# Kernel optimization log

Hardware: AMD Instinct MI355X
Metric: run time of the kernel (lower is better)

Reference implementation:

```python
import jax, jax.numpy as jnp
import numpy as np

SCALES = (4, 8, 8)
PAD = 2
TOTAL = 256  # prod(SCALES) == frame shift
INDENT = PAD * TOTAL
BN_EPS = 1e-3  # keras BatchNormalization default


def _bn(x, g, b, m, v):
    return (x - m) * jax.lax.rsqrt(v + BN_EPS) * g + b


def _conv1d_valid(x, w):
    # x: [B, T, Cin], w: [K, Cin, Cout]
    return jax.lax.conv_general_dilated(x, w, (1,), 'VALID',
                                         dimension_numbers=('NWC', 'WIO', 'NWC'))


def _mel_conv_same(x, w):
    # per-mel-bin shared 1D conv along time. x: [B, T, M], w: [K]
    B, T, M = x.shape
    lhs = x.transpose(0, 2, 1).reshape(B * M, T, 1)
    rhs = w.reshape(-1, 1, 1)
    y = jax.lax.conv_general_dilated(lhs, rhs, (1,), 'SAME',
                                     dimension_numbers=('NWC', 'WIO', 'NWC'))
    return y.reshape(B, M, T).transpose(0, 2, 1)


def _gru(x, Wx, Wh, bx, bh):
    # keras GRUCell (reset_after=True): gate order z, r, h; h' = z*h + (1-z)*hh
    xp = x @ Wx + bx  # [B, T, 3H], input projection hoisted out of the scan
    H = Wh.shape[0]
    h0 = jnp.zeros((x.shape[0], H), x.dtype)

    def step(h, xt):
        rp = h @ Wh + bh
        xz, xr, xh = jnp.split(xt, 3, axis=-1)
        rz, rr, rh = jnp.split(rp, 3, axis=-1)
        z = jax.nn.sigmoid(xz + rz)
        r = jax.nn.sigmoid(xr + rr)
        hh = jnp.tanh(xh + r * rh)
        hn = z * h + (1.0 - z) * hh
        return hn, hn

    _, ys = jax.lax.scan(step, h0, xp.transpose(1, 0, 2))
    return ys.transpose(1, 0, 2)


def setup_inputs() -> dict:
    key = jax.random.key(0)
    ks = iter(jax.random.split(key, 64))
    B, T_MEL, M, C, H, R = 4, 44, 80, 128, 512, 10
    T_UP = TOTAL * (T_MEL - 2 * PAD)  # 10240
    s = 0.05
    d = {}
    d['audios'] = jax.random.normal(next(ks), (B, T_UP + 1), jnp.float32)
    d['mels'] = jax.random.normal(next(ks), (B, T_MEL, M), jnp.float32)
    d['w_mel0'] = jnp.full((2 * SCALES[0] + 1,), 1.0 / (2 * SCALES[0] + 1), jnp.float32)
    d['w_mel1'] = jnp.full((2 * SCALES[1] + 1,), 1.0 / (2 * SCALES[1] + 1), jnp.float32)
    d['w_mel2'] = jnp.full((2 * SCALES[2] + 1,), 1.0 / (2 * SCALES[2] + 1), jnp.float32)
    d['mr_conv0_w'] = jax.random.normal(next(ks), (5, M, C), jnp.float32) * s
    d['mr_bn0_g'] = jax.random.uniform(next(ks), (C,), jnp.float32, 0.5, 1.5)
    d['mr_bn0_b'] = jax.random.normal(next(ks), (C,), jnp.float32) * s
    d['mr_bn0_m'] = jnp.zeros((C,), jnp.float32)
    d['mr_bn0_v'] = jnp.ones((C,), jnp.float32)
    d['r_w1'] = jax.random.normal(next(ks), (R, C, C), jnp.float32) * s
    d['r_bn1_g'] = jax.random.uniform(next(ks), (R, C), jnp.float32, 0.5, 1.5)
    d['r_bn1_b'] = jax.random.normal(next(ks), (R, C), jnp.float32) * s
    d['r_bn1_m'] = jnp.zeros((R, C), jnp.float32)
    d['r_bn1_v'] = jnp.ones((R, C), jnp.float32)
    d['r_w2'] = jax.random.normal(next(ks), (R, C, C), jnp.float32) * s
    d['r_bn2_g'] = jax.random.uniform(next(ks), (R, C), jnp.float32, 0.5, 1.5)
    d['r_bn2_b'] = jax.random.normal(next(ks), (R, C), jnp.float32) * s
    d['r_bn2_m'] = jnp.zeros((R, C), jnp.float32)
    d['r_bn2_v'] = jnp.ones((R, C), jnp.float32)
    d['mr_out_w'] = jax.random.normal(next(ks), (C, C), jnp.float32) * s
    d['mr_out_b'] = jnp.zeros((C,), jnp.float32)
    A4 = C // 4  # 32
    d['Wi'] = jax.random.normal(next(ks), (1 + M + A4, H), jnp.float32) * s
    d['bi'] = jnp.zeros((H,), jnp.float32)
    d['Wx0'] = jax.random.normal(next(ks), (H, 3 * H), jnp.float32) * s
    d['Wh0'] = jax.random.normal(next(ks), (H, 3 * H), jnp.float32) * s
    d['bx0'] = jnp.zeros((3 * H,), jnp.float32)
    d['bh0'] = jnp.zeros((3 * H,), jnp.float32)
    d['Wx1'] = jax.random.normal(next(ks), (H + A4, 3 * H), jnp.float32) * s
    d['Wh1'] = jax.random.normal(next(ks), (H, 3 * H), jnp.float32) * s
    d['bx1'] = jnp.zeros((3 * H,), jnp.float32)
    d['bh1'] = jnp.zeros((3 * H,), jnp.float32)
    d['Wd0'] = jax.random.normal(next(ks), (H + A4, H), jnp.float32) * s
    d['bd0'] = jnp.zeros((H,), jnp.float32)
    d['Wd1'] = jax.random.normal(next(ks), (H + A4, H), jnp.float32) * s
    d['bd1'] = jnp.zeros((H,), jnp.float32)
    d['Wp'] = jax.random.normal(next(ks), (H, 30), jnp.float32) * s
    d['bp'] = jnp.zeros((30,), jnp.float32)
    return d


def reference(audios, mels, w_mel0, w_mel1, w_mel2,
              mr_conv0_w, mr_bn0_g, mr_bn0_b, mr_bn0_m, mr_bn0_v,
              r_w1, r_bn1_g, r_bn1_b, r_bn1_m, r_bn1_v,
              r_w2, r_bn2_g, r_bn2_b, r_bn2_m, r_bn2_v,
              mr_out_w, mr_out_b, Wi, bi,
              Wx0, Wh0, bx0, bh0, Wx1, Wh1, bx1, bh1,
              Wd0, bd0, Wd1, bd1, Wp, bp):
    # ---- UpsampleNet mel branch: nearest upsample + smoothing conv per scale ----
    x = mels
    for w, scale in zip((w_mel0, w_mel1, w_mel2), SCALES):
        x = jnp.repeat(x, scale, axis=1)
        x = _mel_conv_same(x, w)
    mels_up = x[:, INDENT:-INDENT, :]  # [B, T_up, 80]

    # ---- UpsampleNet aux branch: MelResNet (inference BN) + nearest upsample ----
    a = jax.nn.relu(_bn(_conv1d_valid(mels, mr_conv0_w),
                        mr_bn0_g, mr_bn0_b, mr_bn0_m, mr_bn0_v))
    for i in range(r_w1.shape[0]):
        y = jax.nn.relu(_bn(a @ r_w1[i], r_bn1_g[i], r_bn1_b[i], r_bn1_m[i], r_bn1_v[i]))
        y = _bn(y @ r_w2[i], r_bn2_g[i], r_bn2_b[i], r_bn2_m[i], r_bn2_v[i])
        a = a + y
    a = a @ mr_out_w + mr_out_b
    aux = jnp.repeat(a, TOTAL, axis=1)  # [B, T_up, 128]
    a0, a1, a2, a3 = jnp.split(aux, 4, axis=-1)

    # ---- WaveRNN teacher-forced trunk ----
    x = jnp.concatenate([audios[:, :-1, None], mels_up, a0], axis=-1)
    x = x @ Wi + bi  # [B, T_up, 512]
    x = _gru(x, Wx0, Wh0, bx0, bh0) + x
    x = _gru(jnp.concatenate([x, a1], axis=-1), Wx1, Wh1, bx1, bh1) + x
    x = jax.nn.relu(jnp.concatenate([x, a2], axis=-1) @ Wd0 + bd0) + x
    x = jax.nn.relu(jnp.concatenate([x, a3], axis=-1) @ Wd1 + bd1) + x
    logits = x @ Wp + bp  # [B, T_up, 30] (MoL parameters)
    return logits
```

## Files before the change

kernel.cpp:

```cpp
#include <hip/hip_runtime.h>
#include <hip/hip_bf16.h>

#define T_SEQ 10240
#define GRU_W 8

typedef short bf16x8 __attribute__((ext_vector_type(8)));
typedef float f32x4 __attribute__((ext_vector_type(4)));

__device__ __forceinline__ float bf2f(unsigned short u) {
    return __uint_as_float(((unsigned int)u) << 16);
}

__global__ void upsample_kernel(const float* __restrict__ in, float* __restrict__ out,
                                const float* __restrict__ wk,
                                int B, int Tin, int Tout, int shift, int taps)
{
    int idx = blockIdx.x * blockDim.x + threadIdx.x;
    int total = B * Tout * 80;
    if (idx >= total) return;
    int m = idx % 80;
    int r = idx / 80;
    int t = r % Tout;
    int b = r / Tout;
    int s = taps >> 1;
    float acc = 0.f;
    for (int d = -s; d <= s; ++d) {
        int i = t + d;
        if (i >= 0 && i < Tout)
            acc += in[((size_t)b * Tin + (i >> shift)) * 80 + m] * wk[d + s];
    }
    out[idx] = acc;
}

__global__ __launch_bounds__(128) void conv0_kernel(
    const float* __restrict__ mels, const float* __restrict__ w,
    const float* __restrict__ g, const float* __restrict__ b,
    const float* __restrict__ m_, const float* __restrict__ v_,
    float* __restrict__ a)
{
    __shared__ float xin[400];
    int bt = blockIdx.x;
    int bb = bt / 40, t = bt % 40;
    int c = threadIdx.x;
    for (int idx = c; idx < 400; idx += 128)
        xin[idx] = mels[((size_t)bb * 44 + t + idx / 80) * 80 + (idx % 80)];
    __syncthreads();
    float s = 0.f;
    for (int q = 0; q < 400; ++q) s += xin[q] * w[q * 128 + c];
    s = (s - m_[c]) * rsqrtf(v_[c] + 1e-3f) * g[c] + b[c];
    a[bt * 128 + c] = fmaxf(s, 0.f);
}

__global__ __launch_bounds__(128) void resblock_kernel(
    const float* __restrict__ W1, const float* __restrict__ W2,
    const float* __restrict__ g1, const float* __restrict__ b1,
    const float* __restrict__ m1, const float* __restrict__ v1,
    const float* __restrict__ g2, const float* __restrict__ b2,
    const float* __restrict__ m2, const float* __restrict__ v2,
    float* __restrict__ a)
{
    __shared__ float ain[128], y1[128];
    int tok = blockIdx.x;
    int c = threadIdx.x;
    ain[c] = a[tok * 128 + c];
    __syncthreads();
    float s = 0.f;
    #pragma unroll 8
    for (int k = 0; k < 128; ++k) s += ain[k] * W1[k * 128 + c];
    s = (s - m1[c]) * rsqrtf(v1[c] + 1e-3f) * g1[c] + b1[c];
    y1[c] = fmaxf(s, 0.f);
    __syncthreads();
    float s2 = 0.f;
    #pragma unroll 8
    for (int k = 0; k < 128; ++k) s2 += y1[k] * W2[k * 128 + c];
    s2 = (s2 - m2[c]) * rsqrtf(v2[c] + 1e-3f) * g2[c] + b2[c];
    a[tok * 128 + c] = ain[c] + s2;
}

__global__ __launch_bounds__(128) void outmat_kernel(
    const float* __restrict__ W, const float* __restrict__ bias,
    const float* __restrict__ a, float* __restrict__ out)
{
    __shared__ float ain[128];
    int tok = blockIdx.x;
    int c = threadIdx.x;
    ain[c] = a[tok * 128 + c];
    __syncthreads();
    float s = 0.f;
    #pragma unroll 8
    for (int k = 0; k < 128; ++k) s += ain[k] * W[k * 128 + c];
    out[tok * 128 + c] = s + bias[c];
}

__device__ __forceinline__ float fetchA(int mode, int row, int k, int K,
    const float* audio, const float* melsup, const float* cond, const float* xA)
{
    if (k >= K) return 0.f;
    int b = row / T_SEQ;
    int t = row - b * T_SEQ;
    if (mode == 0) {
        if (k == 0) return audio[(size_t)b * (T_SEQ + 1) + t];
        if (k < 81) return melsup[((size_t)b * 11264 + 512 + t) * 80 + (k - 1)];
        return cond[((size_t)b * 40 + (t >> 8)) * 128 + (k - 81)];
    }
    if (k < 512) return xA[(size_t)row * 512 + k];
    int co = (mode == 2) ? 32 : (mode == 3) ? 64 : 96;
    return cond[((size_t)b * 40 + (t >> 8)) * 128 + co + (k - 512)];
}

__global__ __launch_bounds__(256) void gemm_big(
    int mode, int N, int K,
    const float* __restrict__ W, const float* __restrict__ bias1,
    const float* __restrict__ bias2,
    const float* __restrict__ audio, const float* __restrict__ melsup,
    const float* __restrict__ cond, const float* __restrict__ xA,
    const float* __restrict__ resid, float* __restrict__ outF,
    __hip_bfloat16* __restrict__ outB)
{
    __shared__ float As[16][68];
    __shared__ float Bs[16][68];
    const int tid = threadIdx.x;
    const int row0 = blockIdx.y * 64;
    const int col0 = blockIdx.x * 64;
    const int tx = tid & 15, ty = tid >> 4;
    float acc[4][4] = {};
    const int nkt = (K + 15) >> 4;
    for (int kt = 0; kt < nkt; ++kt) {
        const int kb = kt << 4;
        #pragma unroll
        for (int l = 0; l < 4; ++l) {
            int k = (tid >> 6) + l * 4;
            int m = tid & 63;
            float bv = 0.f;
            if (kb + k < K) bv = W[(size_t)(kb + k) * N + col0 + m];
            Bs[k][m] = bv;
        }
        if (mode != 0) {
            int m = tid >> 2, kq = tid & 3;
            int row = row0 + m;
            int k = kb + kq * 4;
            if (k + 3 < 512) {
                float4 v = *reinterpret_cast<const float4*>(xA + (size_t)row * 512 + k);
                As[kq * 4 + 0][m] = v.x; As[kq * 4 + 1][m] = v.y;
                As[kq * 4 + 2][m] = v.z; As[kq * 4 + 3][m] = v.w;
            } else {
                #pragma unroll
                for (int i = 0; i < 4; ++i)
                    As[kq * 4 + i][m] = fetchA(mode, row, k + i, K, audio, melsup, cond, xA);
            }
        } else {
            #pragma unroll
            for (int l = 0; l < 4; ++l) {
                int k = (tid >> 6) + l * 4;
                int m = tid & 63;
                As[k][m] = fetchA(0, row0 + m, kb + k, K, audio, melsup, cond, xA);
            }
        }
        __syncthreads();
        #pragma unroll
        for (int k = 0; k < 16; ++k) {
            float a0 = As[k][(ty << 2) + 0], a1 = As[k][(ty << 2) + 1];
            float a2 = As[k][(ty << 2) + 2], a3 = As[k][(ty << 2) + 3];
            float b0 = Bs[k][(tx << 2) + 0], b1 = Bs[k][(tx << 2) + 1];
            float b2 = Bs[k][(tx << 2) + 2], b3 = Bs[k][(tx << 2) + 3];
            acc[0][0] += a0 * b0; acc[0][1] += a0 * b1; acc[0][2] += a0 * b2; acc[0][3] += a0 * b3;
            acc[1][0] += a1 * b0; acc[1][1] += a1 * b1; acc[1][2] += a1 * b2; acc[1][3] += a1 * b3;
            acc[2][0] += a2 * b0; acc[2][1] += a2 * b1; acc[2][2] += a2 * b2; acc[2][3] += a2 * b3;
            acc[3][0] += a3 * b0; acc[3][1] += a3 * b1; acc[3][2] += a3 * b2; acc[3][3] += a3 * b3;
        }
        __syncthreads();
    }
    #pragma unroll
    for (int i = 0; i < 4; ++i) {
        int row = row0 + (ty << 2) + i;
        #pragma unroll
        for (int jt = 0; jt < 4; ++jt) {
            int col = col0 + (tx << 2) + jt;
            float v = acc[i][jt] + bias1[col];
            if (bias2 && col < 1024) v += bias2[col];
            if (mode == 0) {
                outF[(size_t)row * N + col] = v;
            } else if (mode <= 2) {
                outB[(size_t)row * 1536 + col] = __float2bfloat16(v);
            } else {
                v = fmaxf(v, 0.f) + resid[(size_t)row * 512 + col];
                outF[(size_t)row * 512 + col] = v;
            }
        }
    }
}

__global__ __launch_bounds__(256) void pack_wh_kernel(const float* __restrict__ Wh,
                                                      unsigned short* __restrict__ out)
{
    int gid = blockIdx.x * 256 + threadIdx.x;
    int l = gid & 63;
    int idx = gid >> 6;
    int kt = idx & 15; idx >>= 4;
    int g = idx % 3;
    int ww = idx / 3;
    int wg = ww >> 2, w = ww & 3;
    int n = g * 512 + wg * 64 + w * 16 + (l & 15);
    int k0 = kt * 32 + (l >> 4) * 8;
    unsigned short* dst = out + (size_t)gid * 8;
    #pragma unroll
    for (int i = 0; i < 8; ++i) {
        __hip_bfloat16 hv = __float2bfloat16(Wh[(size_t)(k0 + i) * 1536 + n]);
        dst[i] = *reinterpret_cast<unsigned short*>(&hv);
    }
}

__global__ __launch_bounds__(256, 1) void gru_mfma8(
    const unsigned short* __restrict__ wpack,
    const float* __restrict__ bh,
    const __hip_bfloat16* __restrict__ xp,
    float* __restrict__ xio,
    unsigned int* __restrict__ hpair,
    int T)
{
    __shared__ alignas(16) unsigned short h_sh[2][16 * 512];

    const int tid = threadIdx.x;
    const int wg = blockIdx.x;
    const int w = tid >> 6;
    const int l = tid & 63;

    bf16x8 wf[3][16];
    {
        const bf16x8* wp = reinterpret_cast<const bf16x8*>(wpack);
        const int wbase = (wg * 4 + w) * 3 * 1024;
        #pragma unroll
        for (int g = 0; g < 3; ++g)
            #pragma unroll
            for (int kt = 0; kt < 16; ++kt)
                wf[g][kt] = wp[wbase + (g * 16 + kt) * 64 + l];
    }

    {
        uint4* z = reinterpret_cast<uint4*>(&h_sh[0][0]);
        #pragma unroll
        for (int i = 0; i < 8; ++i) z[tid + 256 * i] = make_uint4(0, 0, 0, 0);
    }

    const int j = wg * 64 + w * 16 + (l & 15);
    const float bhh = bh[1024 + j];
    float hprev[4] = {0.f, 0.f, 0.f, 0.f};
    float xz_c[4], xr_c[4], xh_c[4], xv_c[4];
    if (l < 16) {
        #pragma unroll
        for (int b = 0; b < 4; ++b) {
            const size_t rb = (size_t)b * T;
            xz_c[b] = bf2f(*reinterpret_cast<const unsigned short*>(xp + rb * 1536 + j));
            xr_c[b] = bf2f(*reinterpret_cast<const unsigned short*>(xp + rb * 1536 + 512 + j));
            xh_c[b] = bf2f(*reinterpret_cast<const unsigned short*>(xp + rb * 1536 + 1024 + j));
            xv_c[b] = xio[rb * 512 + j];
        }
    }
    __syncthreads();

    const unsigned long long* hp64 = reinterpret_cast<const unsigned long long*>(hpair);
    const int pb = tid >> 6;
    const int pchunk = (tid & 63) ^ (pb & 7);

    for (int t = 0; t < T; ++t) {
        const int cur = t & 1, nxt = cur ^ 1;

        const unsigned long long* src = hp64 + (size_t)cur * 1024 + tid * 4;
        const unsigned tg = (unsigned)t & 0xffffu;
        unsigned long long u0 = __hip_atomic_load(src + 0, __ATOMIC_RELAXED, __HIP_MEMORY_SCOPE_AGENT);
        unsigned long long u1 = __hip_atomic_load(src + 1, __ATOMIC_RELAXED, __HIP_MEMORY_SCOPE_AGENT);
        unsigned long long u2 = __hip_atomic_load(src + 2, __ATOMIC_RELAXED, __HIP_MEMORY_SCOPE_AGENT);
        unsigned long long u3 = __hip_atomic_load(src + 3, __ATOMIC_RELAXED, __HIP_MEMORY_SCOPE_AGENT);
        while ((((unsigned)(u0 >> 16) & 0xffffu) != tg) | ((unsigned)(u0 >> 48) != tg) |
               (((unsigned)(u1 >> 16) & 0xffffu) != tg) | ((unsigned)(u1 >> 48) != tg) |
               (((unsigned)(u2 >> 16) & 0xffffu) != tg) | ((unsigned)(u2 >> 48) != tg) |
               (((unsigned)(u3 >> 16) & 0xffffu) != tg) | ((unsigned)(u3 >> 48) != tg)) {
            __builtin_amdgcn_s_sleep(1);
            u0 = __hip_atomic_load(src + 0, __ATOMIC_RELAXED, __HIP_MEMORY_SCOPE_AGENT);
            u1 = __hip_atomic_load(src + 1, __ATOMIC_RELAXED, __HIP_MEMORY_SCOPE_AGENT);
            u2 = __hip_atomic_load(src + 2, __ATOMIC_RELAXED, __HIP_MEMORY_SCOPE_AGENT);
            u3 = __hip_atomic_load(src + 3, __ATOMIC_RELAXED, __HIP_MEMORY_SCOPE_AGENT);
        }
        {
            uint4 wv;
            wv.x = (unsigned)(u0 & 0xffffull) | ((unsigned)((u0 >> 32) & 0xffffull) << 16);
            wv.y = (unsigned)(u1 & 0xffffull) | ((unsigned)((u1 >> 32) & 0xffffull) << 16);
            wv.z = (unsigned)(u2 & 0xffffull) | ((unsigned)((u2 >> 32) & 0xffffull) << 16);
            wv.w = (unsigned)(u3 & 0xffffull) | ((unsigned)((u3 >> 32) & 0xffffull) << 16);
            *reinterpret_cast<uint4*>(
                reinterpret_cast<char*>(&h_sh[cur][0]) + pb * 1024 + pchunk * 16) = wv;
        }
        __syncthreads();

        f32x4 acc0 = {0, 0, 0, 0}, acc1 = {0, 0, 0, 0}, acc2 = {0, 0, 0, 0};
        const int rb = l & 15, q = l >> 4;
        const char* hb = reinterpret_cast<const char*>(&h_sh[cur][0]);
        #pragma unroll
        for (int kt = 0; kt < 16; ++kt) {
            bf16x8 afr = *reinterpret_cast<const bf16x8*>(
                hb + rb * 1024 + ((((kt * 4 + q) ^ (rb & 7))) << 4));
            acc0 = __builtin_amdgcn_mfma_f32_16x16x32_bf16(afr, wf[0][kt], acc0, 0, 0, 0);
            acc1 = __builtin_amdgcn_mfma_f32_16x16x32_bf16(afr, wf[1][kt], acc1, 0, 0, 0);
            acc2 = __builtin_amdgcn_mfma_f32_16x16x32_bf16(afr, wf[2][kt], acc2, 0, 0, 0);
        }

        if (l < 16) {
            float hn[4];
            #pragma unroll
            for (int b = 0; b < 4; ++b) {
                float z = 1.f / (1.f + __expf(-(xz_c[b] + acc0[b])));
                float r = 1.f / (1.f + __expf(-(xr_c[b] + acc1[b])));
                float e2 = __expf(-2.f * (xh_c[b] + r * (acc2[b] + bhh)));
                float hh = (1.f - e2) / (1.f + e2);
                hn[b] = z * hprev[b] + (1.f - z) * hh;
                hprev[b] = hn[b];
            }
            if (t + 1 < T) {
                const unsigned ptag = (unsigned)((t + 1) & 0xffff) << 16;
                #pragma unroll
                for (int b = 0; b < 4; ++b) {
                    __hip_bfloat16 hb16 = __float2bfloat16(hn[b]);
                    __hip_atomic_store(hpair + (size_t)nxt * 2048 + b * 512 + j,
                                       ptag | (unsigned)*reinterpret_cast<unsigned short*>(&hb16),
                                       __ATOMIC_RELAXED, __HIP_MEMORY_SCOPE_AGENT);
                }
            }
            #pragma unroll
            for (int b = 0; b < 4; ++b)
                xio[((size_t)b * T + t) * 512 + j] = xv_c[b] + hn[b];
            if (t + 1 < T) {
                #pragma unroll
                for (int b = 0; b < 4; ++b) {
                    const size_t rb2 = (size_t)b * T + t + 1;
                    xz_c[b] = bf2f(*reinterpret_cast<const unsigned short*>(xp + rb2 * 1536 + j));
                    xr_c[b] = bf2f(*reinterpret_cast<const unsigned short*>(xp + rb2 * 1536 + 512 + j));
                    xh_c[b] = bf2f(*reinterpret_cast<const unsigned short*>(xp + rb2 * 1536 + 1024 + j));
                    xv_c[b] = xio[rb2 * 512 + j];
                }
            }
        }
    }
}

__global__ __launch_bounds__(256) void wp_kernel(
    const float* __restrict__ x, const float* __restrict__ Wp,
    const float* __restrict__ bp, float* __restrict__ out)
{
    int r = threadIdx.x >> 5, c = threadIdx.x & 31;
    size_t row = (size_t)blockIdx.x * 8 + r;
    if (c >= 30) return;
    const float* xr = x + row * 512;
    float acc = 0.f;
    #pragma unroll 8
    for (int k = 0; k < 512; ++k) acc += xr[k] * Wp[k * 30 + c];
    out[row * 30 + c] = acc + bp[c];
}

extern "C" void kernel_launch(void* const* d_in, const int* in_sizes, int n_in,
                              void* d_out, int out_size, void* d_ws, size_t ws_size,
                              hipStream_t stream)
{
    const float* audios = (const float*)d_in[0];
    const float* mels   = (const float*)d_in[1];
    const float* w_mel0 = (const float*)d_in[2];
    const float* w_mel1 = (const float*)d_in[3];
    const float* w_mel2 = (const float*)d_in[4];
    const float* conv0w = (const float*)d_in[5];
    const float* bn0g = (const float*)d_in[6];
    const float* bn0b = (const float*)d_in[7];
    const float* bn0m = (const float*)d_in[8];
    const float* bn0v = (const float*)d_in[9];
    const float* r_w1   = (const float*)d_in[10];
    const float* r_bn1g = (const float*)d_in[11];
    const float* r_bn1b = (const float*)d_in[12];
    const float* r_bn1m = (const float*)d_in[13];
    const float* r_bn1v = (const float*)d_in[14];
    const float* r_w2   = (const float*)d_in[15];
    const float* r_bn2g = (const float*)d_in[16];
    const float* r_bn2b = (const float*)d_in[17];
    const float* r_bn2m = (const float*)d_in[18];
    const float* r_bn2v = (const float*)d_in[19];
    const float* mr_out_w = (const float*)d_in[20];
    const float* mr_out_b = (const float*)d_in[21];
    const float* Wi = (const float*)d_in[22];
    const float* bi = (const float*)d_in[23];
    const float* Wx0 = (const float*)d_in[24];
    const float* Wh0 = (const float*)d_in[25];
    const float* bx0 = (const float*)d_in[26];
    const float* bh0 = (const float*)d_in[27];
    const float* Wx1 = (const float*)d_in[28];
    const float* Wh1 = (const float*)d_in[29];
    const float* bx1 = (const float*)d_in[30];
    const float* bh1 = (const float*)d_in[31];
    const float* Wd0 = (const float*)d_in[32];
    const float* bd0 = (const float*)d_in[33];
    const float* Wd1 = (const float*)d_in[34];
    const float* bd1 = (const float*)d_in[35];
    const float* Wp = (const float*)d_in[36];
    const float* bp = (const float*)d_in[37];

    char* ws = (char*)d_ws;
    size_t off = 0;
    auto alloc = [&](size_t n) { size_t r = off; off += (n + 255) & ~(size_t)255; return r; };
    const size_t M = 4 * (size_t)T_SEQ;
    size_t xp_off = alloc(M * 1536 * 2);
    size_t x_off  = alloc(M * 512 * 4);
    size_t s1_off = alloc((size_t)4 * 176 * 80 * 4);
    size_t s2_off = alloc((size_t)4 * 1408 * 80 * 4);
    size_t s3_off = alloc((size_t)4 * 11264 * 80 * 4);
    size_t ca_off = alloc((size_t)160 * 128 * 4);
    size_t cf_off = alloc((size_t)160 * 128 * 4);
    size_t wp0_off = alloc((size_t)98304 * 8 * 2);
    size_t wp1_off = alloc((size_t)98304 * 8 * 2);
    size_t hp_off  = alloc(2 * 2048 * 4);

    __hip_bfloat16* xp = (__hip_bfloat16*)(ws + xp_off);
    float* x3   = (float*)(ws + xp_off);
    float* xbuf = (float*)(ws + x_off);
    float* st1  = (float*)(ws + s1_off);
    float* st2  = (float*)(ws + s2_off);
    float* st3  = (float*)(ws + s3_off);
    float* conda = (float*)(ws + ca_off);
    float* condf = (float*)(ws + cf_off);
    unsigned short* wpack0 = (unsigned short*)(ws + wp0_off);
    unsigned short* wpack1 = (unsigned short*)(ws + wp1_off);
    unsigned int* hpair = (unsigned int*)(ws + hp_off);
    float* outp = (float*)d_out;

    pack_wh_kernel<<<384, 256, 0, stream>>>(Wh0, wpack0);
    pack_wh_kernel<<<384, 256, 0, stream>>>(Wh1, wpack1);

    {
        int tot1 = 4 * 176 * 80;
        upsample_kernel<<<(tot1 + 255) / 256, 256, 0, stream>>>(mels, st1, w_mel0, 4, 44, 176, 2, 9);
        int tot2 = 4 * 1408 * 80;
        upsample_kernel<<<(tot2 + 255) / 256, 256, 0, stream>>>(st1, st2, w_mel1, 4, 176, 1408, 3, 17);
        int tot3 = 4 * 11264 * 80;
        upsample_kernel<<<(tot3 + 255) / 256, 256, 0, stream>>>(st2, st3, w_mel2, 4, 1408, 11264, 3, 17);
    }
    conv0_kernel<<<160, 128, 0, stream>>>(mels, conv0w, bn0g, bn0b, bn0m, bn0v, conda);
    for (int i = 0; i < 10; ++i) {
        resblock_kernel<<<160, 128, 0, stream>>>(
            r_w1 + (size_t)i * 128 * 128, r_w2 + (size_t)i * 128 * 128,
            r_bn1g + i * 128, r_bn1b + i * 128, r_bn1m + i * 128, r_bn1v + i * 128,
            r_bn2g + i * 128, r_bn2b + i * 128, r_bn2m + i * 128, r_bn2v + i * 128,
            conda);
    }
    outmat_kernel<<<160, 128, 0, stream>>>(mr_out_w, mr_out_b, conda, condf);

    dim3 blk(256);
    gemm_big<<<dim3(8, 640), blk, 0, stream>>>(0, 512, 113, Wi, bi, nullptr,
        audios, st3, condf, nullptr, nullptr, xbuf, nullptr);
    gemm_big<<<dim3(24, 640), blk, 0, stream>>>(1, 1536, 512, Wx0, bx0, bh0,
        nullptr, nullptr, condf, xbuf, nullptr, nullptr, xp);
    hipMemsetAsync(ws + hp_off, 0, 2 * 2048 * 4, stream);
    gru_mfma8<<<GRU_W, 256, 0, stream>>>(wpack0, bh0, xp, xbuf, hpair, T_SEQ);
    gemm_big<<<dim3(24, 640), blk, 0, stream>>>(2, 1536, 544, Wx1, bx1, bh1,
        nullptr, nullptr, condf, xbuf, nullptr, nullptr, xp);
    hipMemsetAsync(ws + hp_off, 0, 2 * 2048 * 4, stream);
    gru_mfma8<<<GRU_W, 256, 0, stream>>>(wpack1, bh1, xp, xbuf, hpair, T_SEQ);
    gemm_big<<<dim3(8, 640), blk, 0, stream>>>(3, 512, 544, Wd0, bd0, nullptr,
        nullptr, nullptr, condf, xbuf, xbuf, x3, nullptr);
    gemm_big<<<dim3(8, 640), blk, 0, stream>>>(4, 512, 544, Wd1, bd1, nullptr,
        nullptr, nullptr, condf, x3, x3, xbuf, nullptr);
    wp_kernel<<<5120, 256, 0, stream>>>(xbuf, Wp, bp, outp);
}
```

Before: 48.35 ms.

## Add producer warp prefetching GRU input projections into shared memory

Adds a fifth warp to the recurrent GRU kernel that loads the next timestep's input-projection and residual values into a triple-buffered shared-memory ring. The four compute warps then read these from LDS instead of doing per-step global loads after writing the hidden state. This aims to take global-load latency off the serial per-step critical path. The cost is an extra warp in every block-wide barrier, so a slow prefetch can still stall the step.

```diff
diff --git a/kernel.cpp b/kernel.cpp
--- a/kernel.cpp
+++ b/kernel.cpp
@@ -210,7 +210,7 @@
     }
 }
 
-__global__ __launch_bounds__(256, 1) void gru_mfma8(
+__global__ __launch_bounds__(320, 1) void gru_mfma8(
     const unsigned short* __restrict__ wpack,
     const float* __restrict__ bh,
     const __hip_bfloat16* __restrict__ xp,
@@ -219,6 +219,8 @@
     int T)
 {
     __shared__ alignas(16) unsigned short h_sh[2][16 * 512];
+    __shared__ alignas(16) unsigned short xp_sh[3][4][3][64];
+    __shared__ alignas(16) float xv_sh[3][4][64];
 
     const int tid = threadIdx.x;
     const int wg = blockIdx.x;
@@ -226,7 +228,7 @@
     const int l = tid & 63;
 
     bf16x8 wf[3][16];
-    {
+    if (w < 4) {
         const bf16x8* wp = reinterpret_cast<const bf16x8*>(wpack);
         const int wbase = (wg * 4 + w) * 3 * 1024;
         #pragma unroll
@@ -238,22 +240,31 @@
 
     {
         uint4* z = reinterpret_cast<uint4*>(&h_sh[0][0]);
+        for (int i = tid; i < 2048; i += 320) z[i] = make_uint4(0, 0, 0, 0);
+    }
+
+    const int j = wg * 64 + w * 16 + (l & 15);
+    float bhh = 0.f;
+    float hprev[4] = {0.f, 0.f, 0.f, 0.f};
+    if (w < 4 && l < 16) bhh = bh[1024 + j];
+
+    if (w == 4) {
         #pragma unroll
-        for (int i = 0; i < 8; ++i) z[tid + 256 * i] = make_uint4(0, 0, 0, 0);
-    }
-
-    const int j = wg * 64 + w * 16 + (l & 15);
-    const float bhh = bh[1024 + j];
-    float hprev[4] = {0.f, 0.f, 0.f, 0.f};
-    float xz_c[4], xr_c[4], xh_c[4], xv_c[4];
-    if (l < 16) {
-        #pragma unroll
-        for (int b = 0; b < 4; ++b) {
-            const size_t rb = (size_t)b * T;
-            xz_c[b] = bf2f(*reinterpret_cast<const unsigned short*>(xp + rb * 1536 + j));
-            xr_c[b] = bf2f(*reinterpret_cast<const unsigned short*>(xp + rb * 1536 + 512 + j));
-            xh_c[b] = bf2f(*reinterpret_cast<const unsigned short*>(xp + rb * 1536 + 1024 + j));
-            xv_c[b] = xio[rb * 512 + j];
+        for (int k = 0; k < 3; ++k) {
+            int c = l + 64 * k;
+            if (c < 96) {
+                int s = c >> 3, sub = c & 7;
+                int b = s / 3, g = s % 3;
+                uint4 v = *reinterpret_cast<const uint4*>(
+                    reinterpret_cast<const unsigned short*>(xp) +
+                    (size_t)b * T * 1536 + g * 512 + wg * 64 + sub * 8);
+                *reinterpret_cast<uint4*>(&xp_sh[0][b][g][sub * 8]) = v;
+            } else if (c < 160) {
+                int q = c - 96, b = q >> 4, sub = q & 15;
+                float4 v = *reinterpret_cast<const float4*>(
+                    xio + (size_t)b * T * 512 + wg * 64 + sub * 4);
+                *reinterpret_cast<float4*>(&xv_sh[0][b][sub * 4]) = v;
+            }
         }
     }
     __syncthreads();
@@ -264,24 +275,25 @@
 
     for (int t = 0; t < T; ++t) {
         const int cur = t & 1, nxt = cur ^ 1;
-
-        const unsigned long long* src = hp64 + (size_t)cur * 1024 + tid * 4;
-        const unsigned tg = (unsigned)t & 0xffffu;
-        unsigned long long u0 = __hip_atomic_load(src + 0, __ATOMIC_RELAXED, __HIP_MEMORY_SCOPE_AGENT);
-        unsigned long long u1 = __hip_atomic_load(src + 1, __ATOMIC_RELAXED, __HIP_MEMORY_SCOPE_AGENT);
-        unsigned long long u2 = __hip_atomic_load(src + 2, __ATOMIC_RELAXED, __HIP_MEMORY_SCOPE_AGENT);
-        unsigned long long u3 = __hip_atomic_load(src + 3, __ATOMIC_RELAXED, __HIP_MEMORY_SCOPE_AGENT);
-        while ((((unsigned)(u0 >> 16) & 0xffffu) != tg) | ((unsigned)(u0 >> 48) != tg) |
-               (((unsigned)(u1 >> 16) & 0xffffu) != tg) | ((unsigned)(u1 >> 48) != tg) |
-               (((unsigned)(u2 >> 16) & 0xffffu) != tg) | ((unsigned)(u2 >> 48) != tg) |
-               (((unsigned)(u3 >> 16) & 0xffffu) != tg) | ((unsigned)(u3 >> 48) != tg)) {
-            __builtin_amdgcn_s_sleep(1);
-            u0 = __hip_atomic_load(src + 0, __ATOMIC_RELAXED, __HIP_MEMORY_SCOPE_AGENT);
-            u1 = __hip_atomic_load(src + 1, __ATOMIC_RELAXED, __HIP_MEMORY_SCOPE_AGENT);
-            u2 = __hip_atomic_load(src + 2, __ATOMIC_RELAXED, __HIP_MEMORY_SCOPE_AGENT);
-            u3 = __hip_atomic_load(src + 3, __ATOMIC_RELAXED, __HIP_MEMORY_SCOPE_AGENT);
-        }
-        {
+        const int bu = t % 3;
+
+        if (w < 4) {
+            const unsigned long long* src = hp64 + (size_t)cur * 1024 + tid * 4;
+            const unsigned tg = (unsigned)t & 0xffffu;
+            unsigned long long u0 = __hip_atomic_load(src + 0, __ATOMIC_RELAXED, __HIP_MEMORY_SCOPE_AGENT);
+            unsigned long long u1 = __hip_atomic_load(src + 1, __ATOMIC_RELAXED, __HIP_MEMORY_SCOPE_AGENT);
+            unsigned long long u2 = __hip_atomic_load(src + 2, __ATOMIC_RELAXED, __HIP_MEMORY_SCOPE_AGENT);
+            unsigned long long u3 = __hip_atomic_load(src + 3, __ATOMIC_RELAXED, __HIP_MEMORY_SCOPE_AGENT);
+            while ((((unsigned)(u0 >> 16) & 0xffffu) != tg) | ((unsigned)(u0 >> 48) != tg) |
+                   (((unsigned)(u1 >> 16) & 0xffffu) != tg) | ((unsigned)(u1 >> 48) != tg) |
+                   (((unsigned)(u2 >> 16) & 0xffffu) != tg) | ((unsigned)(u2 >> 48) != tg) |
+                   (((unsigned)(u3 >> 16) & 0xffffu) != tg) | ((unsigned)(u3 >> 48) != tg)) {
+                __builtin_amdgcn_s_sleep(1);
+                u0 = __hip_atomic_load(src + 0, __ATOMIC_RELAXED, __HIP_MEMORY_SCOPE_AGENT);
+                u1 = __hip_atomic_load(src + 1, __ATOMIC_RELAXED, __HIP_MEMORY_SCOPE_AGENT);
+                u2 = __hip_atomic_load(src + 2, __ATOMIC_RELAXED, __HIP_MEMORY_SCOPE_AGENT);
+                u3 = __hip_atomic_load(src + 3, __ATOMIC_RELAXED, __HIP_MEMORY_SCOPE_AGENT);
+            }
             uint4 wv;
             wv.x = (unsigned)(u0 & 0xffffull) | ((unsigned)((u0 >> 32) & 0xffffull) << 16);
             wv.y = (unsigned)(u1 & 0xffffull) | ((unsigned)((u1 >> 32) & 0xffffull) << 16);
@@ -289,54 +301,71 @@
             wv.w = (unsigned)(u3 & 0xffffull) | ((unsigned)((u3 >> 32) & 0xffffull) << 16);
             *reinterpret_cast<uint4*>(
                 reinterpret_cast<char*>(&h_sh[cur][0]) + pb * 1024 + pchunk * 16) = wv;
+        } else {
+            if (t + 1 < T) {
+                const int bn = (t + 1) % 3;
+                #pragma unroll
+                for (int k = 0; k < 3; ++k) {
+                    int c = l + 64 * k;
+                    if (c < 96) {
+                        int s = c >> 3, sub = c & 7;
+                        int b = s / 3, g = s % 3;
+                        uint4 v = *reinterpret_cast<const uint4*>(
+                            reinterpret_cast<const unsigned short*>(xp) +
+                            ((size_t)b * T + t + 1) * 1536 + g * 512 + wg * 64 + sub * 8);
+                        *reinterpret_cast<uint4*>(&xp_sh[bn][b][g][sub * 8]) = v;
+                    } else if (c < 160) {
+                        int q = c - 96, b = q >> 4, sub = q & 15;
+                        float4 v = *reinterpret_cast<const float4*>(
+                            xio + ((size_t)b * T + t + 1) * 512 + wg * 64 + sub * 4);
+                        *reinterpret_cast<float4*>(&xv_sh[bn][b][sub * 4]) = v;
+                    }
+                }
+            }
         }
         __syncthreads();
 
-        f32x4 acc0 = {0, 0, 0, 0}, acc1 = {0, 0, 0, 0}, acc2 = {0, 0, 0, 0};
-        const int rb = l & 15, q = l >> 4;
-        const char* hb = reinterpret_cast<const char*>(&h_sh[cur][0]);
-        #pragma unroll
-        for (int kt = 0; kt < 16; ++kt) {
-            bf16x8 afr = *reinterpret_cast<const bf16x8*>(
-                hb + rb * 1024 + ((((kt * 4 + q) ^ (rb & 7))) << 4));
-            acc0 = __builtin_amdgcn_mfma_f32_16x16x32_bf16(afr, wf[0][kt], acc0, 0, 0, 0);
-            acc1 = __builtin_amdgcn_mfma_f32_16x16x32_bf16(afr, wf[1][kt], acc1, 0, 0, 0);
-            acc2 = __builtin_amdgcn_mfma_f32_16x16x32_bf16(afr, wf[2][kt], acc2, 0, 0, 0);
-        }
-
-        if (l < 16) {
-            float hn[4];
+        if (w < 4) {
+            f32x4 acc0 = {0, 0, 0, 0}, acc1 = {0, 0, 0, 0}, acc2 = {0, 0, 0, 0};
+            const int rb = l & 15, q = l >> 4;
+            const char* hb = reinterpret_cast<const char*>(&h_sh[cur][0]);
             #pragma unroll
-            for (int b = 0; b < 4; ++b) {
-                float z = 1.f / (1.f + __expf(-(xz_c[b] + acc0[b])));
-                float r = 1.f / (1.f + __expf(-(xr_c[b] + acc1[b])));
-                float e2 = __expf(-2.f * (xh_c[b] + r * (acc2[b] + bhh)));
-                float hh = (1.f - e2) / (1.f + e2);
-                hn[b] = z * hprev[b] + (1.f - z) * hh;
-                hprev[b] = hn[b];
-            }
-            if (t + 1 < T) {
-                const unsigned ptag = (unsigned)((t + 1) & 0xffff) << 16;
+            for (int kt = 0; kt < 16; ++kt) {
+                bf16x8 afr = *reinterpret_cast<const bf16x8*>(
+                    hb + rb * 1024 + ((((kt * 4 + q) ^ (rb & 7))) << 4));
+                acc0 = __builtin_amdgcn_mfma_f32_16x16x32_bf16(afr, wf[0][kt], acc0, 0, 0, 0);
+                acc1 = __builtin_amdgcn_mfma_f32_16x16x32_bf16(afr, wf[1][kt], acc1, 0, 0, 0);
+                acc2 = __builtin_amdgcn_mfma_f32_16x16x32_bf16(afr, wf[2][kt], acc2, 0, 0, 0);
+            }
+
+            if (l < 16) {
+                const int jl = w * 16 + l;
+                float hn[4];
                 #pragma unroll
                 for (int b = 0; b < 4; ++b) {
-                    __hip_bfloat16 hb16 = __float2bfloat16(hn[b]);
-                    __hip_atomic_store(hpair + (size_t)nxt * 2048 + b * 512 + j,
-                                       ptag | (unsigned)*reinterpret_cast<unsigned short*>(&hb16),
-                                       __ATOMIC_RELAXED, __HIP_MEMORY_SCOPE_AGENT);
+                    float xz = bf2f(xp_sh[bu][b][0][jl]);
+                    float xr = bf2f(xp_sh[bu][b][1][jl]);
+                    float xh = bf2f(xp_sh[bu][b][2][jl]);
+                    float z = 1.f / (1.f + __expf(-(xz + acc0[b])));
+                    float r = 1.f / (1.f + __expf(-(xr + acc1[b])));
+                    float e2 = __expf(-2.f * (xh + r * (acc2[b] + bhh)));
+                    float hh = (1.f - e2) / (1.f + e2);
+                    hn[b] = z * hprev[b] + (1.f - z) * hh;
+                    hprev[b] = hn[b];
                 }
-            }
-            #pragma unroll
-            for (int b = 0; b < 4; ++b)
-                xio[((size_t)b * T + t) * 512 + j] = xv_c[b] + hn[b];
-            if (t + 1 < T) {
+                if (t + 1 < T) {
+                    const unsigned ptag = (unsigned)((t + 1) & 0xffff) << 16;
+                    #pragma unroll
+                    for (int b = 0; b < 4; ++b) {
+                        __hip_bfloat16 hb16 = __float2bfloat16(hn[b]);
+                        __hip_atomic_store(hpair + (size_t)nxt * 2048 + b * 512 + j,
+                                           ptag | (unsigned)*reinterpret_cast<unsigned short*>(&hb16),
+                                           __ATOMIC_RELAXED, __HIP_MEMORY_SCOPE_AGENT);
+                    }
+                }
                 #pragma unroll
-                for (int b = 0; b < 4; ++b) {
-                    const size_t rb2 = (size_t)b * T + t + 1;
-                    xz_c[b] = bf2f(*reinterpret_cast<const unsigned short*>(xp + rb2 * 1536 + j));
-                    xr_c[b] = bf2f(*reinterpret_cast<const unsigned short*>(xp + rb2 * 1536 + 512 + j));
-                    xh_c[b] = bf2f(*reinterpret_cast<const unsigned short*>(xp + rb2 * 1536 + 1024 + j));
-                    xv_c[b] = xio[rb2 * 512 + j];
-                }
+                for (int b = 0; b < 4; ++b)
+                    xio[((size_t)b * T + t) * 512 + j] = xv_sh[bu][b][jl] + hn[b];
             }
         }
     }
@@ -454,11 +483,11 @@
     gemm_big<<<dim3(24, 640), blk, 0, stream>>>(1, 1536, 512, Wx0, bx0, bh0,
         nullptr, nullptr, condf, xbuf, nullptr, nullptr, xp);
     hipMemsetAsync(ws + hp_off, 0, 2 * 2048 * 4, stream);
-    gru_mfma8<<<GRU_W, 256, 0, stream>>>(wpack0, bh0, xp, xbuf, hpair, T_SEQ);
+    gru_mfma8<<<GRU_W, 320, 0, stream>>>(wpack0, bh0, xp, xbuf, hpair, T_SEQ);
     gemm_big<<<dim3(24, 640), blk, 0, stream>>>(2, 1536, 544, Wx1, bx1, bh1,
         nullptr, nullptr, condf, xbuf, nullptr, nullptr, xp);
     hipMemsetAsync(ws + hp_off, 0, 2 * 2048 * 4, stream);
-    gru_mfma8<<<GRU_W, 256, 0, stream>>>(wpack1, bh1, xp, xbuf, hpair, T_SEQ);
+    gru_mfma8<<<GRU_W, 320, 0, stream>>>(wpack1, bh1, xp, xbuf, hpair, T_SEQ);
     gemm_big<<<dim3(8, 640), blk, 0, stream>>>(3, 512, 544, Wd0, bd0, nullptr,
         nullptr, nullptr, condf, xbuf, xbuf, x3, nullptr);
     gemm_big<<<dim3(8, 640), blk, 0, stream>>>(4, 512, 544, Wd1, bd1, nullptr,
```

New measurement: 60.04 ms. 1.24x slower.
